# Kernel tuning notes

Hardware: AMD Instinct MI355X
Metric: run time of the kernel (lower is better)

The kernel has to match this reference:

```python
import jax, jax.numpy as jnp
import numpy as np

T, B, D, H = 2048, 64, 256, 256
DROPOUT = 0.3  # eval-mode recurrent dropout -> scalar scale (1 - dropout) on gate inputs


def setup_inputs() -> dict:
    key = jax.random.key(0)
    ks = jax.random.split(key, 5)
    x = jax.random.normal(ks[0], (T, B, D), dtype=jnp.float32)
    # variable sequence lengths, sorted descending (PackedSequence convention), min 1
    lengths = jnp.sort(jax.random.randint(ks[1], (B,), 1, T + 1))[::-1].astype(jnp.int64)
    # stacked gate weights, gate order i, f, c(g), o (matches bias_ih slicing)
    W = jax.random.normal(ks[2], (4 * H, D), dtype=jnp.float32) / np.sqrt(D).astype(np.float32)
    U = jax.random.normal(ks[3], (4 * H, H), dtype=jnp.float32) / np.sqrt(H).astype(np.float32)
    b_ih = jnp.zeros((4 * H,), jnp.float32).at[H:2 * H].set(1.0)  # forget-gate bias = 1
    b_hh = jnp.zeros((4 * H,), jnp.float32)
    return {"x": x, "lengths": lengths, "W": W, "U": U, "b_ih": b_ih, "b_hh": b_hh}


def reference(x, lengths, W, U, b_ih, b_hh):
    p = jnp.float32(1.0 - DROPOUT)
    Tn, Bn, _ = x.shape
    Hn = U.shape[1]
    b = b_ih + b_hh  # fused bias, shape [4H]
    t_idx = jnp.arange(Tn)

    def step(carry, inp):
        h, c = carry
        x_t, t = inp                      # x_t: [B, D]
        active = (t < lengths)[:, None]   # [B, 1] bool: sequence still running
        gates = (x_t * p) @ W.T + (h * p) @ U.T + b  # [B, 4H]
        i_g, f_g, g_g, o_g = jnp.split(gates, 4, axis=-1)
        i_t = jax.nn.sigmoid(i_g)
        f_t = jax.nn.sigmoid(f_g)
        o_t = jax.nn.sigmoid(o_g)
        c_new = f_t * c + i_t * jnp.tanh(g_g)
        h_new = o_t * jnp.tanh(c_new)
        # inactive rows keep their final state (packed-sequence semantics)
        h = jnp.where(active, h_new, h)
        c = jnp.where(active, c_new, c)
        out = jnp.where(active, h_new, jnp.float32(0.0))
        return (h, c), out

    init = (jnp.zeros((Bn, Hn), x.dtype), jnp.zeros((Bn, Hn), x.dtype))
    (h_n, c_n), outputs = jax.lax.scan(step, init, (x, t_idx))
    return outputs, h_n, c_n
```

## Files before the change

kernel.cpp:

```cpp
#include <hip/hip_runtime.h>


#define T_STEPS 2048
#define BATCH   64
#define DIM     256
#define HID     256
#define PKEEP   0.7f
#define RPG     16
#define TCHUNK  32
#define REGION_U32 (RPG * HID * 2)
#define PLANE_U32  (4 * REGION_U32)
#define XEL     (T_STEPS * BATCH * DIM)

typedef __attribute__((ext_vector_type(8))) short s16x8;
typedef __attribute__((ext_vector_type(4))) float f32x4;
typedef __attribute__((ext_vector_type(4))) unsigned int u32x4;
typedef __attribute__((ext_vector_type(2))) unsigned int u32x2;
typedef unsigned int u32;
typedef unsigned short u16;

#define HBUF_OFF 4096
#define BIG_OFF  (1 << 20)
#define ZERO_INTS (2 * PLANE_U32)

#define HISEL 0x07060302u
#define LOSEL 0x05040100u

__device__ __forceinline__ u16 f2bf_rne(float f) {
  unsigned x = __float_as_uint(f);
  return (u16)((x + 0x7fffu + ((x >> 16) & 1u)) >> 16);
}
__device__ __forceinline__ float bf2f(u16 u) { return __uint_as_float(((unsigned)u) << 16); }
__device__ __forceinline__ float sigm(float v) { return 1.0f / (1.0f + __expf(-v)); }
__device__ __forceinline__ float tanh_f(float v) {
  float e = __expf(-2.0f * fabsf(v));
  float r = (1.0f - e) / (1.0f + e);
  return v < 0.0f ? -r : r;
}
__device__ __forceinline__ u32 packbf(float v) {
  u32 uh = __float_as_uint(v) & 0xFFFF0000u;
  u32 lo = (u32)f2bf_rne(v - __uint_as_float(uh));
  return uh | lo;
}
__device__ __forceinline__ void dev_st_u32x2(u32* p, u32x2 v) {
  asm volatile("global_store_dwordx2 %0, %1, off sc0 sc1" :: "v"(p), "v"(v) : "memory");
}
__device__ __forceinline__ void gload_lds16(const u32* g, u32* lds) {
  __builtin_amdgcn_global_load_lds(
      (const __attribute__((address_space(1))) u32*)g,
      (__attribute__((address_space(3))) u32*)lds, 16, 0, 0);
}
__device__ __forceinline__ void unpack8(u32x4 a, u32x4 b, s16x8& hi, s16x8& lo) {
  u32x4 H, L;
  H[0] = __builtin_amdgcn_perm(a[1], a[0], HISEL);
  H[1] = __builtin_amdgcn_perm(a[3], a[2], HISEL);
  H[2] = __builtin_amdgcn_perm(b[1], b[0], HISEL);
  H[3] = __builtin_amdgcn_perm(b[3], b[2], HISEL);
  L[0] = __builtin_amdgcn_perm(a[1], a[0], LOSEL);
  L[1] = __builtin_amdgcn_perm(a[3], a[2], LOSEL);
  L[2] = __builtin_amdgcn_perm(b[1], b[0], LOSEL);
  L[3] = __builtin_amdgcn_perm(b[3], b[2], LOSEL);
  hi = __builtin_bit_cast(s16x8, H);
  lo = __builtin_bit_cast(s16x8, L);
}
__device__ __forceinline__ void xpose4(f32x4& a, bool b2, bool b3) {
  {
    int t0 = __builtin_amdgcn_ds_swizzle(__float_as_int(a[1]), 0x101F);
    int u0 = __builtin_amdgcn_ds_swizzle(__float_as_int(a[0]), 0x101F);
    int t1 = __builtin_amdgcn_ds_swizzle(__float_as_int(a[3]), 0x101F);
    int u1 = __builtin_amdgcn_ds_swizzle(__float_as_int(a[2]), 0x101F);
    float A0 = b2 ? __int_as_float(t0) : a[0];
    float A1 = b2 ? a[1] : __int_as_float(u0);
    float A2 = b2 ? __int_as_float(t1) : a[2];
    float A3 = b2 ? a[3] : __int_as_float(u1);
    a[0] = A0; a[1] = A1; a[2] = A2; a[3] = A3;
  }
  {
    int t0 = __builtin_amdgcn_ds_swizzle(__float_as_int(a[2]), 0x201F);
    int u0 = __builtin_amdgcn_ds_swizzle(__float_as_int(a[0]), 0x201F);
    int t1 = __builtin_amdgcn_ds_swizzle(__float_as_int(a[3]), 0x201F);
    int u1 = __builtin_amdgcn_ds_swizzle(__float_as_int(a[1]), 0x201F);
    float A0 = b3 ? __int_as_float(t0) : a[0];
    float A2 = b3 ? a[2] : __int_as_float(u0);
    float A1 = b3 ? __int_as_float(t1) : a[1];
    float A3 = b3 ? a[3] : __int_as_float(u1);
    a[0] = A0; a[1] = A1; a[2] = A2; a[3] = A3;
  }
}

__global__ void lstm_zero_ws(u32* __restrict__ p) {
  int i = blockIdx.x * 256 + threadIdx.x;
  if (i < ZERO_INTS) p[i] = 0;
}

__global__ void lstm_xpack(const float* __restrict__ x, u32* __restrict__ xpk) {
  long i = ((long)blockIdx.x * 256 + threadIdx.x) * 4;
  if (i >= (long)XEL) return;
  f32x4 v = *(const f32x4*)(x + i);
  u32x4 o;
#pragma unroll
  for (int e = 0; e < 4; ++e) o[e] = packbf(v[e] * PKEEP);
  *(u32x4*)(xpk + i) = o;
}

__global__ __launch_bounds__(256, 1) void lstm_gxp14(
    const float* __restrict__ x, const float* __restrict__ W,
    u32* __restrict__ Gxb) {
  const int tid = threadIdx.x;
  const int n = blockIdx.x & 15, m = (blockIdx.x >> 4) & 3;
  const int tc = blockIdx.x >> 6;
  const int t0 = tc * TCHUNK;
  const int lane = tid & 63, wave = tid >> 6;
  const int n16 = lane & 15, kgrp = lane >> 4;

  const int ghc_w = n * 16 + wave * 4 + (n16 & 3);
  const int grow = (n16 >> 2) * HID + ghc_w;
  s16x8 BWh[8], BWl[8];
#pragma unroll
  for (int ks = 0; ks < 8; ++ks) {
    const int base = grow * DIM + ks * 32 + kgrp * 8;
#pragma unroll
    for (int e = 0; e < 8; ++e) {
      float wv = W[base + e];
      u16 wh = f2bf_rne(wv);
      BWh[ks][e] = (short)wh;
      BWl[ks][e] = (short)f2bf_rne(wv - bf2f(wh));
    }
  }

  const bool b2 = (lane >> 2) & 1, b3 = (lane >> 3) & 1;
  const int row_l = kgrp * 4 + (n16 >> 2);
  const int gb = m * RPG + row_l;

  __shared__ u32 xstage[2][RPG * HID];

  {
    const int R = wave * 4;
    const long tb = (long)t0 * (BATCH * DIM) + (long)(m * RPG) * DIM;
#pragma unroll
    for (int r = 0; r < 4; ++r) {
      const long src = tb + (long)(R + r) * DIM + 4 * (lane ^ ((R + r) & 15));
      gload_lds16((const u32*)x + src, &xstage[0][(R + r) * HID]);
    }
  }

  for (int ti = 0; ti < TCHUNK; ++ti) {
    const int t = t0 + ti, par = ti & 1;
    asm volatile("s_waitcnt vmcnt(0)" ::: "memory");
    __builtin_amdgcn_sched_barrier(0);
    __syncthreads();

    const int swz = n16 << 4;
    f32x4 ax = {0.f, 0.f, 0.f, 0.f};
#pragma unroll
    for (int ks = 0; ks < 8; ++ks) {
      const int bb = n16 * 1024 + (kgrp * 8 + ks * 32) * 4;
      f32x4 f0 = *(const f32x4*)((const char*)xstage[par] + (bb ^ swz));
      f32x4 f1 = *(const f32x4*)((const char*)xstage[par] + ((bb + 16) ^ swz));
      s16x8 Xh, Xl;
#pragma unroll
      for (int e = 0; e < 8; ++e) {
        float v = (e < 4 ? f0[e] : f1[e - 4]) * PKEEP;
        unsigned hb = __float_as_uint(v) & 0xFFFF0000u;
        Xh[e] = (short)(hb >> 16);
        Xl[e] = (short)(u16)(__float_as_uint(v - __uint_as_float(hb)) >> 16);
      }
      ax = __builtin_amdgcn_mfma_f32_16x16x32_bf16(Xh, BWh[ks], ax, 0, 0, 0);
      ax = __builtin_amdgcn_mfma_f32_16x16x32_bf16(Xl, BWh[ks], ax, 0, 0, 0);
      ax = __builtin_amdgcn_mfma_f32_16x16x32_bf16(Xh, BWl[ks], ax, 0, 0, 0);
    }

    f32x4 g4 = ax;
    xpose4(g4, b2, b3);

    u32x2 pv;
    pv[0] = ((u32)f2bf_rne(g4[0]) << 16) | (u32)f2bf_rne(g4[1]);
    pv[1] = ((u32)f2bf_rne(g4[2]) << 16) | (u32)f2bf_rne(g4[3]);
    *(u32x2*)(Gxb + ((long)(t * BATCH + gb)) * 512 + ghc_w * 2) = pv;

    if (ti + 1 < TCHUNK) {
      const int R = wave * 4;
      const long tb = (long)(t + 1) * (BATCH * DIM) + (long)(m * RPG) * DIM;
#pragma unroll
      for (int r = 0; r < 4; ++r) {
        const long src = tb + (long)(R + r) * DIM + 4 * (lane ^ ((R + r) & 15));
        gload_lds16((const u32*)x + src, &xstage[par ^ 1][(R + r) * HID]);
      }
    }
  }
}

__global__ __launch_bounds__(256, 1) void lstm_recur_v14(
    const float* __restrict__ x, const int* __restrict__ lens,
    const float* __restrict__ W, const float* __restrict__ U,
    const float* __restrict__ bih, const float* __restrict__ bhh,
    float* __restrict__ out, u32* __restrict__ hbuf, const u32* __restrict__ Gxb) {
  const int wg = blockIdx.x, tid = threadIdx.x;
  const int m = wg >> 4, n = wg & 15;
  const int lane = tid & 63, wave = tid >> 6;
  const int n16 = lane & 15, kgrp = lane >> 4;

  const int ghc_w = n * 16 + wave * 4 + (n16 & 3);
  const int grow = (n16 >> 2) * HID + ghc_w;
  s16x8 BUh[8], BUl[8];
#pragma unroll
  for (int ks = 0; ks < 8; ++ks) {
    const int base = grow * DIM + ks * 32 + kgrp * 8;
#pragma unroll
    for (int e = 0; e < 8; ++e) {
      float uv = U[base + e];
      u16 uh = f2bf_rne(uv);
      BUh[ks][e] = (short)uh;
      BUl[ks][e] = (short)f2bf_rne(uv - bf2f(uh));
    }
  }

  const bool b2 = (lane >> 2) & 1, b3 = (lane >> 3) & 1;
  const int row_l = kgrp * 4 + (n16 >> 2);
  const int gb = m * RPG + row_l;
  const float bi  = bih[0 * HID + ghc_w] + bhh[0 * HID + ghc_w];
  const float bfo = bih[1 * HID + ghc_w] + bhh[1 * HID + ghc_w];
  const float bg  = bih[2 * HID + ghc_w] + bhh[2 * HID + ghc_w];
  const float bo  = bih[3 * HID + ghc_w] + bhh[3 * HID + ghc_w];
  const int len = lens[gb];
  float hreg = 0.0f, creg = 0.0f;

  const int rh = tid >> 7, p = tid & 127;
  __shared__ u32 hstage[2][RPG * HID];

  u32x2 gxu = *(const u32x2*)(Gxb + ((long)gb) * 512 + ghc_w * 2);

  for (int t = 0; t < T_STEPS; ++t) {
    const int par = t & 1;

    u32x4 P[8];
    {
      const u32* rb = hbuf + par * PLANE_U32 + m * REGION_U32 + rh * (8 * 512) + p * 4;
      for (;;) {
#pragma unroll
        for (int j = 0; j < 8; ++j)
          asm volatile("global_load_dwordx4 %0, %1, off sc0 sc1"
                       : "=v"(P[j]) : "v"(rb + j * 512) : "memory");
        asm volatile("s_waitcnt vmcnt(0)" ::: "memory");
        if (t == 0) break;
        bool stale = false;
#pragma unroll
        for (int j = 0; j < 8; ++j)
          stale |= (P[j][1] != (u32)t) || (P[j][3] != (u32)t);
        if (!__any(stale)) break;
      }
    }
    __builtin_amdgcn_sched_barrier(0);

#pragma unroll
    for (int j = 0; j < 8; ++j) {
      const int row = rh * 8 + j;
      const int byte = (row * 1024 + p * 8) ^ (row << 4);
      u32x2 v = {P[j][0], P[j][2]};
      *(u32x2*)((char*)hstage[par] + byte) = v;
    }
    __syncthreads();

    const int swz = n16 << 4;
    f32x4 ah = {0.f, 0.f, 0.f, 0.f};
#pragma unroll
    for (int ks = 0; ks < 8; ++ks) {
      const int bb = n16 * 1024 + (kgrp * 8 + ks * 32) * 4;
      u32x4 h0 = *(const u32x4*)((const char*)hstage[par] + (bb ^ swz));
      u32x4 h1 = *(const u32x4*)((const char*)hstage[par] + ((bb + 16) ^ swz));
      s16x8 Hh, Hl;
      unpack8(h0, h1, Hh, Hl);
      ah = __builtin_amdgcn_mfma_f32_16x16x32_bf16(Hh, BUh[ks], ah, 0, 0, 0);
      ah = __builtin_amdgcn_mfma_f32_16x16x32_bf16(Hl, BUh[ks], ah, 0, 0, 0);
      ah = __builtin_amdgcn_mfma_f32_16x16x32_bf16(Hh, BUl[ks], ah, 0, 0, 0);
    }

    f32x4 g4 = ah;
    xpose4(g4, b2, b3);
    float gi = g4[0] + __uint_as_float(gxu[0] & 0xFFFF0000u) + bi;
    float gf = g4[1] + __uint_as_float(gxu[0] << 16)          + bfo;
    float gg = g4[2] + __uint_as_float(gxu[1] & 0xFFFF0000u) + bg;
    float go = g4[3] + __uint_as_float(gxu[1] << 16)          + bo;
    float it = sigm(gi), ft = sigm(gf), ot = sigm(go);
    float gt = tanh_f(gg);
    float cnew = ft * creg + it * gt;
    float hnew = ot * tanh_f(cnew);
    const bool act = (t < len);
    if (act) { creg = cnew; hreg = hnew; }
    {
      u32x2 pv = {packbf(hreg * PKEEP), (u32)(t + 1)};
      dev_st_u32x2(hbuf + (par ^ 1) * PLANE_U32 + m * REGION_U32 + row_l * 512 + ghc_w * 2, pv);
    }

    if (t + 1 < T_STEPS)
      gxu = *(const u32x2*)(Gxb + ((long)((t + 1) * BATCH + gb)) * 512 + ghc_w * 2);
    out[(long)t * (BATCH * HID) + gb * HID + ghc_w] = act ? hnew : 0.0f;

    asm volatile("s_waitcnt vmcnt(0)" ::: "memory");
    __builtin_amdgcn_sched_barrier(0);
  }

  out[(long)T_STEPS * (BATCH * HID) + gb * HID + ghc_w] = hreg;
  out[(long)T_STEPS * (BATCH * HID) + BATCH * HID + gb * HID + ghc_w] = creg;
}

template <int MODE>
__device__ __forceinline__ void recur_body8(
    const float* __restrict__ x, const int* __restrict__ lens,
    const float* __restrict__ W, const float* __restrict__ U,
    const float* __restrict__ bih, const float* __restrict__ bhh,
    float* __restrict__ out, u32* __restrict__ hbuf, const u32* __restrict__ xpk) {
  const int wg = blockIdx.x, tid = threadIdx.x;
  const int m = wg >> 4, n = wg & 15;
  const int lane = tid & 63, wave = tid >> 6;
  const int n16 = lane & 15, kgrp = lane >> 4;

  const int ghc_w = n * 16 + wave * 4 + (n16 & 3);
  const int grow = (n16 >> 2) * HID + ghc_w;
  s16x8 BUh[8], BUl[8], BWh[8], BWl[8];
#pragma unroll
  for (int ks = 0; ks < 8; ++ks) {
    const int base = grow * DIM + ks * 32 + kgrp * 8;
#pragma unroll
    for (int e = 0; e < 8; ++e) {
      float uv = U[base + e];
      u16 uh = f2bf_rne(uv);
      BUh[ks][e] = (short)uh;
      BUl[ks][e] = (short)f2bf_rne(uv - bf2f(uh));
      float wv = W[base + e];
      u16 wh = f2bf_rne(wv);
      BWh[ks][e] = (short)wh;
      BWl[ks][e] = (short)f2bf_rne(wv - bf2f(wh));
    }
  }

  const bool b2 = (lane >> 2) & 1, b3 = (lane >> 3) & 1;
  const int row_l = kgrp * 4 + (n16 >> 2);
  const int gb = m * RPG + row_l;
  const float bi  = bih[0 * HID + ghc_w] + bhh[0 * HID + ghc_w];
  const float bfo = bih[1 * HID + ghc_w] + bhh[1 * HID + ghc_w];
  const float bg  = bih[2 * HID + ghc_w] + bhh[2 * HID + ghc_w];
  const float bo  = bih[3 * HID + ghc_w] + bhh[3 * HID + ghc_w];
  const int len = lens[gb];
  float hreg = 0.0f, creg = 0.0f;

  const int rh = tid >> 7, p = tid & 127;

  __shared__ u32 hstage[2][RPG * HID];
  __shared__ u32 xstage[2][RPG * HID];

  {
    const int R = wave * 4;
    const long tb = (long)(m * RPG) * DIM;
#pragma unroll
    for (int r = 0; r < 4; ++r) {
      const long src = tb + (long)(R + r) * DIM + 4 * (lane ^ ((R + r) & 15));
      if constexpr (MODE == 0) gload_lds16(xpk + src, &xstage[0][(R + r) * HID]);
      else                     gload_lds16((const u32*)x + src, &xstage[0][(R + r) * HID]);
    }
  }

  for (int t = 0; t < T_STEPS; ++t) {
    const int par = t & 1;
    u32x4 P[8];
    {
      const u32* rb = hbuf + par * PLANE_U32 + m * REGION_U32 + rh * (8 * 512) + p * 4;
      for (;;) {
#pragma unroll
        for (int j = 0; j < 8; ++j)
          asm volatile("global_load_dwordx4 %0, %1, off sc0 sc1"
                       : "=v"(P[j]) : "v"(rb + j * 512) : "memory");
        asm volatile("s_waitcnt vmcnt(0)" ::: "memory");
        if (t == 0) break;
        bool stale = false;
#pragma unroll
        for (int j = 0; j < 8; ++j)
          stale |= (P[j][1] != (u32)t) || (P[j][3] != (u32)t);
        if (!__any(stale)) break;
      }
    }
    __builtin_amdgcn_sched_barrier(0);

#pragma unroll
    for (int j = 0; j < 8; ++j) {
      const int row = rh * 8 + j;
      const int byte = (row * 1024 + p * 8) ^ (row << 4);
      u32x2 v = {P[j][0], P[j][2]};
      *(u32x2*)((char*)hstage[par] + byte) = v;
    }
    __syncthreads();

    const int swz = n16 << 4;
    f32x4 ah = {0.f, 0.f, 0.f, 0.f}, ax = {0.f, 0.f, 0.f, 0.f};
#pragma unroll
    for (int ks = 0; ks < 8; ++ks) {
      const int bb = n16 * 1024 + (kgrp * 8 + ks * 32) * 4;
      u32x4 h0 = *(const u32x4*)((const char*)hstage[par] + (bb ^ swz));
      u32x4 h1 = *(const u32x4*)((const char*)hstage[par] + ((bb + 16) ^ swz));
      s16x8 Hh, Hl, Xh, Xl;
      unpack8(h0, h1, Hh, Hl);
      if constexpr (MODE == 0) {
        u32x4 x0 = *(const u32x4*)((const char*)xstage[par] + (bb ^ swz));
        u32x4 x1 = *(const u32x4*)((const char*)xstage[par] + ((bb + 16) ^ swz));
        unpack8(x0, x1, Xh, Xl);
      } else {
        f32x4 f0 = *(const f32x4*)((const char*)xstage[par] + (bb ^ swz));
        f32x4 f1 = *(const f32x4*)((const char*)xstage[par] + ((bb + 16) ^ swz));
#pragma unroll
        for (int e = 0; e < 8; ++e) {
          float v = (e < 4 ? f0[e] : f1[e - 4]) * PKEEP;
          unsigned hb = __float_as_uint(v) & 0xFFFF0000u;
          Xh[e] = (short)(hb >> 16);
          Xl[e] = (short)(u16)(__float_as_uint(v - __uint_as_float(hb)) >> 16);
        }
      }
      ah = __builtin_amdgcn_mfma_f32_16x16x32_bf16(Hh, BUh[ks], ah, 0, 0, 0);
      ax = __builtin_amdgcn_mfma_f32_16x16x32_bf16(Xh, BWh[ks], ax, 0, 0, 0);
      ah = __builtin_amdgcn_mfma_f32_16x16x32_bf16(Hl, BUh[ks], ah, 0, 0, 0);
      ax = __builtin_amdgcn_mfma_f32_16x16x32_bf16(Xl, BWh[ks], ax, 0, 0, 0);
      ah = __builtin_amdgcn_mfma_f32_16x16x32_bf16(Hh, BUl[ks], ah, 0, 0, 0);
      ax = __builtin_amdgcn_mfma_f32_16x16x32_bf16(Xh, BWl[ks], ax, 0, 0, 0);
    }

    f32x4 g4 = ah + ax;
    xpose4(g4, b2, b3);

    float gi = g4[0] + bi, gf = g4[1] + bfo, gg = g4[2] + bg, go = g4[3] + bo;
    float it = sigm(gi), ft = sigm(gf), ot = sigm(go);
    float gt = tanh_f(gg);
    float cnew = ft * creg + it * gt;
    float hnew = ot * tanh_f(cnew);
    const bool act = (t < len);
    if (act) { creg = cnew; hreg = hnew; }
    {
      u32x2 pv = {packbf(hreg * PKEEP), (u32)(t + 1)};
      dev_st_u32x2(hbuf + (par ^ 1) * PLANE_U32 + m * REGION_U32 + row_l * 512 + ghc_w * 2, pv);
    }

    if (t + 1 < T_STEPS) {
      const int R = wave * 4;
      const long tb = (long)(t + 1) * (BATCH * DIM) + (long)(m * RPG) * DIM;
#pragma unroll
      for (int r = 0; r < 4; ++r) {
        const long src = tb + (long)(R + r) * DIM + 4 * (lane ^ ((R + r) & 15));
        if constexpr (MODE == 0) gload_lds16(xpk + src, &xstage[par ^ 1][(R + r) * HID]);
        else                     gload_lds16((const u32*)x + src, &xstage[par ^ 1][(R + r) * HID]);
      }
    }
    out[(long)t * (BATCH * HID) + gb * HID + ghc_w] = act ? hnew : 0.0f;

    asm volatile("s_waitcnt vmcnt(0)" ::: "memory");
    __builtin_amdgcn_sched_barrier(0);
  }

  out[(long)T_STEPS * (BATCH * HID) + gb * HID + ghc_w] = hreg;
  out[(long)T_STEPS * (BATCH * HID) + BATCH * HID + gb * HID + ghc_w] = creg;
}

#define RECUR_PARAMS                                                          \
  const float* __restrict__ x, const int* __restrict__ lens,                  \
  const float* __restrict__ W, const float* __restrict__ U,                   \
  const float* __restrict__ bih, const float* __restrict__ bhh,               \
  float* __restrict__ out, u32* __restrict__ hbuf, const u32* __restrict__ xpk
#define RECUR_ARGS x, lens, W, U, bih, bhh, out, hbuf, xpk

__global__ __launch_bounds__(256, 1) void lstm_recur_v8_xpk(RECUR_PARAMS) { recur_body8<0>(RECUR_ARGS); }
__global__ __launch_bounds__(256, 1) void lstm_recur_v8_dir(RECUR_PARAMS) { recur_body8<1>(RECUR_ARGS); }

extern "C" void kernel_launch(void* const* d_in, const int* in_sizes, int n_in,
                              void* d_out, int out_size, void* d_ws, size_t ws_size,
                              hipStream_t stream) {
  const float* x   = (const float*)d_in[0];
  const int*   len = (const int*)d_in[1];
  const float* W   = (const float*)d_in[2];
  const float* U   = (const float*)d_in[3];
  const float* bih = (const float*)d_in[4];
  const float* bhh = (const float*)d_in[5];
  float* out = (float*)d_out;
  char*  ws  = (char*)d_ws;
  u32* hbuf = (u32*)(ws + HBUF_OFF);
  char* big = ws + BIG_OFF;

  lstm_zero_ws<<<dim3((ZERO_INTS + 255) / 256), dim3(256), 0, stream>>>(hbuf);

  const size_t need_gx = (size_t)BIG_OFF + (size_t)T_STEPS * BATCH * 512 * 4;
  const size_t need_xp = (size_t)BIG_OFF + (size_t)XEL * 4;
  if (ws_size >= need_gx) {
    u32* Gxb = (u32*)big;
    lstm_gxp14<<<dim3(64 * (T_STEPS / TCHUNK)), dim3(256), 0, stream>>>(x, W, Gxb);
    lstm_recur_v14<<<dim3(64), dim3(256), 0, stream>>>(x, len, W, U, bih, bhh, out, hbuf, Gxb);
  } else if (ws_size >= need_xp) {
    u32* xpk = (u32*)big;
    lstm_xpack<<<dim3(32768), dim3(256), 0, stream>>>(x, xpk);
    lstm_recur_v8_xpk<<<dim3(64), dim3(256), 0, stream>>>(x, len, W, U, bih, bhh, out, hbuf, xpk);
  } else {
    lstm_recur_v8_dir<<<dim3(64), dim3(256), 0, stream>>>(x, len, W, U, bih, bhh, out, hbuf, nullptr);
  }
}
```

Before: 4.975 ms.

## Halve recurrent workgroups by computing two hidden-column tiles per workgroup

The recurrent kernel now runs 32 workgroups instead of 64. Each one handles 32 hidden columns as two interleaved 16-column MFMA tiles, with U held in registers for both tiles. The goal is to cut the number of workgroups taking part in the per-step cross-workgroup h exchange and spin-wait, and to reuse each staged h tile for twice the MFMA work. The cost is doubled register pressure from the weight fragments, plus more serial MFMA and gate work per step on each workgroup.

```diff
diff --git a/kernel.cpp b/kernel.cpp
--- a/kernel.cpp
+++ b/kernel.cpp
@@ -190,45 +190,55 @@
   }
 }
 
-__global__ __launch_bounds__(256, 1) void lstm_recur_v14(
+__global__ __launch_bounds__(256, 1) void lstm_recur_v15(
     const float* __restrict__ x, const int* __restrict__ lens,
     const float* __restrict__ W, const float* __restrict__ U,
     const float* __restrict__ bih, const float* __restrict__ bhh,
     float* __restrict__ out, u32* __restrict__ hbuf, const u32* __restrict__ Gxb) {
   const int wg = blockIdx.x, tid = threadIdx.x;
-  const int m = wg >> 4, n = wg & 15;
+  const int m = wg >> 3, nb = wg & 7;
   const int lane = tid & 63, wave = tid >> 6;
   const int n16 = lane & 15, kgrp = lane >> 4;
 
-  const int ghc_w = n * 16 + wave * 4 + (n16 & 3);
-  const int grow = (n16 >> 2) * HID + ghc_w;
-  s16x8 BUh[8], BUl[8];
+  const int ghc0 = nb * 32 + wave * 4 + (n16 & 3);
+  const int ghc1 = ghc0 + 16;
+  s16x8 BU0h[8], BU0l[8], BU1h[8], BU1l[8];
 #pragma unroll
   for (int ks = 0; ks < 8; ++ks) {
-    const int base = grow * DIM + ks * 32 + kgrp * 8;
+    const int base0 = ((n16 >> 2) * HID + ghc0) * DIM + ks * 32 + kgrp * 8;
+    const int base1 = ((n16 >> 2) * HID + ghc1) * DIM + ks * 32 + kgrp * 8;
 #pragma unroll
     for (int e = 0; e < 8; ++e) {
-      float uv = U[base + e];
-      u16 uh = f2bf_rne(uv);
-      BUh[ks][e] = (short)uh;
-      BUl[ks][e] = (short)f2bf_rne(uv - bf2f(uh));
+      float u0 = U[base0 + e];
+      u16 h0 = f2bf_rne(u0);
+      BU0h[ks][e] = (short)h0;
+      BU0l[ks][e] = (short)f2bf_rne(u0 - bf2f(h0));
+      float u1 = U[base1 + e];
+      u16 h1 = f2bf_rne(u1);
+      BU1h[ks][e] = (short)h1;
+      BU1l[ks][e] = (short)f2bf_rne(u1 - bf2f(h1));
     }
   }
 
   const bool b2 = (lane >> 2) & 1, b3 = (lane >> 3) & 1;
   const int row_l = kgrp * 4 + (n16 >> 2);
   const int gb = m * RPG + row_l;
-  const float bi  = bih[0 * HID + ghc_w] + bhh[0 * HID + ghc_w];
-  const float bfo = bih[1 * HID + ghc_w] + bhh[1 * HID + ghc_w];
-  const float bg  = bih[2 * HID + ghc_w] + bhh[2 * HID + ghc_w];
-  const float bo  = bih[3 * HID + ghc_w] + bhh[3 * HID + ghc_w];
+  const float bi0  = bih[0 * HID + ghc0] + bhh[0 * HID + ghc0];
+  const float bf0  = bih[1 * HID + ghc0] + bhh[1 * HID + ghc0];
+  const float bg0  = bih[2 * HID + ghc0] + bhh[2 * HID + ghc0];
+  const float bo0  = bih[3 * HID + ghc0] + bhh[3 * HID + ghc0];
+  const float bi1  = bih[0 * HID + ghc1] + bhh[0 * HID + ghc1];
+  const float bf1  = bih[1 * HID + ghc1] + bhh[1 * HID + ghc1];
+  const float bg1  = bih[2 * HID + ghc1] + bhh[2 * HID + ghc1];
+  const float bo1  = bih[3 * HID + ghc1] + bhh[3 * HID + ghc1];
   const int len = lens[gb];
-  float hreg = 0.0f, creg = 0.0f;
+  float hreg0 = 0.f, creg0 = 0.f, hreg1 = 0.f, creg1 = 0.f;
 
   const int rh = tid >> 7, p = tid & 127;
   __shared__ u32 hstage[2][RPG * HID];
 
-  u32x2 gxu = *(const u32x2*)(Gxb + ((long)gb) * 512 + ghc_w * 2);
+  u32x2 gxu0 = *(const u32x2*)(Gxb + ((long)gb) * 512 + ghc0 * 2);
+  u32x2 gxu1 = *(const u32x2*)(Gxb + ((long)gb) * 512 + ghc1 * 2);
 
   for (int t = 0; t < T_STEPS; ++t) {
     const int par = t & 1;
@@ -262,7 +272,7 @@
     __syncthreads();
 
     const int swz = n16 << 4;
-    f32x4 ah = {0.f, 0.f, 0.f, 0.f};
+    f32x4 a0 = {0.f, 0.f, 0.f, 0.f}, a1 = {0.f, 0.f, 0.f, 0.f};
 #pragma unroll
     for (int ks = 0; ks < 8; ++ks) {
       const int bb = n16 * 1024 + (kgrp * 8 + ks * 32) * 4;
@@ -270,38 +280,65 @@
       u32x4 h1 = *(const u32x4*)((const char*)hstage[par] + ((bb + 16) ^ swz));
       s16x8 Hh, Hl;
       unpack8(h0, h1, Hh, Hl);
-      ah = __builtin_amdgcn_mfma_f32_16x16x32_bf16(Hh, BUh[ks], ah, 0, 0, 0);
-      ah = __builtin_amdgcn_mfma_f32_16x16x32_bf16(Hl, BUh[ks], ah, 0, 0, 0);
-      ah = __builtin_amdgcn_mfma_f32_16x16x32_bf16(Hh, BUl[ks], ah, 0, 0, 0);
-    }
-
-    f32x4 g4 = ah;
-    xpose4(g4, b2, b3);
-    float gi = g4[0] + __uint_as_float(gxu[0] & 0xFFFF0000u) + bi;
-    float gf = g4[1] + __uint_as_float(gxu[0] << 16)          + bfo;
-    float gg = g4[2] + __uint_as_float(gxu[1] & 0xFFFF0000u) + bg;
-    float go = g4[3] + __uint_as_float(gxu[1] << 16)          + bo;
-    float it = sigm(gi), ft = sigm(gf), ot = sigm(go);
-    float gt = tanh_f(gg);
-    float cnew = ft * creg + it * gt;
-    float hnew = ot * tanh_f(cnew);
+      a0 = __builtin_amdgcn_mfma_f32_16x16x32_bf16(Hh, BU0h[ks], a0, 0, 0, 0);
+      a1 = __builtin_amdgcn_mfma_f32_16x16x32_bf16(Hh, BU1h[ks], a1, 0, 0, 0);
+      a0 = __builtin_amdgcn_mfma_f32_16x16x32_bf16(Hl, BU0h[ks], a0, 0, 0, 0);
+      a1 = __builtin_amdgcn_mfma_f32_16x16x32_bf16(Hl, BU1h[ks], a1, 0, 0, 0);
+      a0 = __builtin_amdgcn_mfma_f32_16x16x32_bf16(Hh, BU0l[ks], a0, 0, 0, 0);
+      a1 = __builtin_amdgcn_mfma_f32_16x16x32_bf16(Hh, BU1l[ks], a1, 0, 0, 0);
+    }
+
     const bool act = (t < len);
-    if (act) { creg = cnew; hreg = hnew; }
+    float hnew0, hnew1;
     {
-      u32x2 pv = {packbf(hreg * PKEEP), (u32)(t + 1)};
-      dev_st_u32x2(hbuf + (par ^ 1) * PLANE_U32 + m * REGION_U32 + row_l * 512 + ghc_w * 2, pv);
-    }
-
-    if (t + 1 < T_STEPS)
-      gxu = *(const u32x2*)(Gxb + ((long)((t + 1) * BATCH + gb)) * 512 + ghc_w * 2);
-    out[(long)t * (BATCH * HID) + gb * HID + ghc_w] = act ? hnew : 0.0f;
+      f32x4 g4 = a0;
+      xpose4(g4, b2, b3);
+      float gi = g4[0] + __uint_as_float(gxu0[0] & 0xFFFF0000u) + bi0;
+      float gf = g4[1] + __uint_as_float(gxu0[0] << 16)          + bf0;
+      float gg = g4[2] + __uint_as_float(gxu0[1] & 0xFFFF0000u) + bg0;
+      float go = g4[3] + __uint_as_float(gxu0[1] << 16)          + bo0;
+      float it = sigm(gi), ft = sigm(gf), ot = sigm(go);
+      float gt = tanh_f(gg);
+      float cnew = ft * creg0 + it * gt;
+      float hn = ot * tanh_f(cnew);
+      if (act) { creg0 = cnew; hreg0 = hn; }
+      hnew0 = hn;
+      u32x2 pv = {packbf(hreg0 * PKEEP), (u32)(t + 1)};
+      dev_st_u32x2(hbuf + (par ^ 1) * PLANE_U32 + m * REGION_U32 + row_l * 512 + ghc0 * 2, pv);
+    }
+    {
+      f32x4 g4 = a1;
+      xpose4(g4, b2, b3);
+      float gi = g4[0] + __uint_as_float(gxu1[0] & 0xFFFF0000u) + bi1;
+      float gf = g4[1] + __uint_as_float(gxu1[0] << 16)          + bf1;
+      float gg = g4[2] + __uint_as_float(gxu1[1] & 0xFFFF0000u) + bg1;
+      float go = g4[3] + __uint_as_float(gxu1[1] << 16)          + bo1;
+      float it = sigm(gi), ft = sigm(gf), ot = sigm(go);
+      float gt = tanh_f(gg);
+      float cnew = ft * creg1 + it * gt;
+      float hn = ot * tanh_f(cnew);
+      if (act) { creg1 = cnew; hreg1 = hn; }
+      hnew1 = hn;
+      u32x2 pv = {packbf(hreg1 * PKEEP), (u32)(t + 1)};
+      dev_st_u32x2(hbuf + (par ^ 1) * PLANE_U32 + m * REGION_U32 + row_l * 512 + ghc1 * 2, pv);
+    }
+
+    if (t + 1 < T_STEPS) {
+      const long gxb = ((long)((t + 1) * BATCH + gb)) * 512;
+      gxu0 = *(const u32x2*)(Gxb + gxb + ghc0 * 2);
+      gxu1 = *(const u32x2*)(Gxb + gxb + ghc1 * 2);
+    }
+    out[(long)t * (BATCH * HID) + gb * HID + ghc0] = act ? hnew0 : 0.0f;
+    out[(long)t * (BATCH * HID) + gb * HID + ghc1] = act ? hnew1 : 0.0f;
 
     asm volatile("s_waitcnt vmcnt(0)" ::: "memory");
     __builtin_amdgcn_sched_barrier(0);
   }
 
-  out[(long)T_STEPS * (BATCH * HID) + gb * HID + ghc_w] = hreg;
-  out[(long)T_STEPS * (BATCH * HID) + BATCH * HID + gb * HID + ghc_w] = creg;
+  out[(long)T_STEPS * (BATCH * HID) + gb * HID + ghc0] = hreg0;
+  out[(long)T_STEPS * (BATCH * HID) + gb * HID + ghc1] = hreg1;
+  out[(long)T_STEPS * (BATCH * HID) + BATCH * HID + gb * HID + ghc0] = creg0;
+  out[(long)T_STEPS * (BATCH * HID) + BATCH * HID + gb * HID + ghc1] = creg1;
 }
 
 template <int MODE>
@@ -488,7 +525,7 @@
   if (ws_size >= need_gx) {
     u32* Gxb = (u32*)big;
     lstm_gxp14<<<dim3(64 * (T_STEPS / TCHUNK)), dim3(256), 0, stream>>>(x, W, Gxb);
-    lstm_recur_v14<<<dim3(64), dim3(256), 0, stream>>>(x, len, W, U, bih, bhh, out, hbuf, Gxb);
+    lstm_recur_v15<<<dim3(32), dim3(256), 0, stream>>>(x, len, W, U, bih, bhh, out, hbuf, Gxb);
   } else if (ws_size >= need_xp) {
     u32* xpk = (u32*)big;
     lstm_xpack<<<dim3(32768), dim3(256), 0, stream>>>(x, xpk);
```

New measurement: 5.859 ms. 17.8% more time.

## Fuse input projection and recurrence into one producer-consumer kernel with flags

Applied to the files above, without the earlier changes.

Replaces the separate input-projection kernel and recurrence kernel with one launch of 128 workgroups. 64 workgroups run the sequential recurrence while 64 producer workgroups compute the W·x gate contributions step by step. The producers signal progress through coherent per-tile flags, so the recurrence starts without waiting for the whole projection pass. The risks are spin-wait latency on the flags, the producers pacing the consumers, and a deadlock if the two roles are not co-resident on the device.

```diff
diff --git a/kernel.cpp b/kernel.cpp
--- a/kernel.cpp
+++ b/kernel.cpp
@@ -7,10 +7,11 @@
 #define HID     256
 #define PKEEP   0.7f
 #define RPG     16
-#define TCHUNK  32
 #define REGION_U32 (RPG * HID * 2)
 #define PLANE_U32  (4 * REGION_U32)
 #define XEL     (T_STEPS * BATCH * DIM)
+#define NH      64
+#define NX      64
 
 typedef __attribute__((ext_vector_type(8))) short s16x8;
 typedef __attribute__((ext_vector_type(4))) float f32x4;
@@ -19,9 +20,10 @@
 typedef unsigned int u32;
 typedef unsigned short u16;
 
-#define HBUF_OFF 4096
+#define XF_OFF   4096
+#define HBUF_OFF 16384
 #define BIG_OFF  (1 << 20)
-#define ZERO_INTS (2 * PLANE_U32)
+#define ZERO_U32 ((HBUF_OFF + 2 * PLANE_U32 * 4) / 4)
 
 #define HISEL 0x07060302u
 #define LOSEL 0x05040100u
@@ -44,6 +46,19 @@
 }
 __device__ __forceinline__ void dev_st_u32x2(u32* p, u32x2 v) {
   asm volatile("global_store_dwordx2 %0, %1, off sc0 sc1" :: "v"(p), "v"(v) : "memory");
+}
+__device__ __forceinline__ void coh_st_i32(int* p, int v) {
+  asm volatile("global_store_dword %0, %1, off sc0 sc1" :: "v"(p), "v"(v) : "memory");
+}
+__device__ __forceinline__ int coh_ld_i32(const int* p) {
+  int v;
+  asm volatile("global_load_dword %0, %1, off sc0 sc1" : "=v"(v) : "v"(p) : "memory");
+  return v;
+}
+__device__ __forceinline__ u32x2 coh_ld_u32x2(const u32* p) {
+  u32x2 v;
+  asm volatile("global_load_dwordx2 %0, %1, off sc0 sc1" : "=v"(v) : "v"(p) : "memory");
+  return v;
 }
 __device__ __forceinline__ void gload_lds16(const u32* g, u32* lds) {
   __builtin_amdgcn_global_load_lds(
@@ -90,7 +105,7 @@
 
 __global__ void lstm_zero_ws(u32* __restrict__ p) {
   int i = blockIdx.x * 256 + threadIdx.x;
-  if (i < ZERO_INTS) p[i] = 0;
+  if (i < ZERO_U32) p[i] = 0;
 }
 
 __global__ void lstm_xpack(const float* __restrict__ x, u32* __restrict__ xpk) {
@@ -103,14 +118,12 @@
   *(u32x4*)(xpk + i) = o;
 }
 
-__global__ __launch_bounds__(256, 1) void lstm_gxp14(
+__device__ __forceinline__ void x_role(
     const float* __restrict__ x, const float* __restrict__ W,
-    u32* __restrict__ Gxb) {
-  const int tid = threadIdx.x;
-  const int n = blockIdx.x & 15, m = (blockIdx.x >> 4) & 3;
-  const int tc = blockIdx.x >> 6;
-  const int t0 = tc * TCHUNK;
-  const int lane = tid & 63, wave = tid >> 6;
+    u32* __restrict__ Gxb, int* __restrict__ xf, u32* smem) {
+  const int bx = blockIdx.x - NH;
+  const int m = bx >> 4, n = bx & 15;
+  const int tid = threadIdx.x, lane = tid & 63, wave = tid >> 6;
   const int n16 = lane & 15, kgrp = lane >> 4;
 
   const int ghc_w = n * 16 + wave * 4 + (n16 & 3);
@@ -127,36 +140,35 @@
       BWl[ks][e] = (short)f2bf_rne(wv - bf2f(wh));
     }
   }
-
   const bool b2 = (lane >> 2) & 1, b3 = (lane >> 3) & 1;
   const int row_l = kgrp * 4 + (n16 >> 2);
   const int gb = m * RPG + row_l;
-
-  __shared__ u32 xstage[2][RPG * HID];
+  int* flagp = xf + (m * 16 + n) * 16;
 
   {
     const int R = wave * 4;
-    const long tb = (long)t0 * (BATCH * DIM) + (long)(m * RPG) * DIM;
+    const long tb = (long)(m * RPG) * DIM;
 #pragma unroll
     for (int r = 0; r < 4; ++r) {
       const long src = tb + (long)(R + r) * DIM + 4 * (lane ^ ((R + r) & 15));
-      gload_lds16((const u32*)x + src, &xstage[0][(R + r) * HID]);
-    }
-  }
-
-  for (int ti = 0; ti < TCHUNK; ++ti) {
-    const int t = t0 + ti, par = ti & 1;
+      gload_lds16((const u32*)x + src, smem + (R + r) * HID);
+    }
+  }
+
+  for (int t = 0; t < T_STEPS; ++t) {
+    const int par = t & 1;
     asm volatile("s_waitcnt vmcnt(0)" ::: "memory");
     __builtin_amdgcn_sched_barrier(0);
     __syncthreads();
 
     const int swz = n16 << 4;
+    const char* xs = (const char*)smem + par * (RPG * HID * 4);
     f32x4 ax = {0.f, 0.f, 0.f, 0.f};
 #pragma unroll
     for (int ks = 0; ks < 8; ++ks) {
       const int bb = n16 * 1024 + (kgrp * 8 + ks * 32) * 4;
-      f32x4 f0 = *(const f32x4*)((const char*)xstage[par] + (bb ^ swz));
-      f32x4 f1 = *(const f32x4*)((const char*)xstage[par] + ((bb + 16) ^ swz));
+      f32x4 f0 = *(const f32x4*)(xs + (bb ^ swz));
+      f32x4 f1 = *(const f32x4*)(xs + ((bb + 16) ^ swz));
       s16x8 Xh, Xl;
 #pragma unroll
       for (int e = 0; e < 8; ++e) {
@@ -172,29 +184,31 @@
 
     f32x4 g4 = ax;
     xpose4(g4, b2, b3);
-
     u32x2 pv;
     pv[0] = ((u32)f2bf_rne(g4[0]) << 16) | (u32)f2bf_rne(g4[1]);
     pv[1] = ((u32)f2bf_rne(g4[2]) << 16) | (u32)f2bf_rne(g4[3]);
-    *(u32x2*)(Gxb + ((long)(t * BATCH + gb)) * 512 + ghc_w * 2) = pv;
-
-    if (ti + 1 < TCHUNK) {
+    dev_st_u32x2(Gxb + ((long)(t * BATCH + gb)) * 512 + ghc_w * 2, pv);
+
+    asm volatile("s_waitcnt vmcnt(0)" ::: "memory");
+    __syncthreads();
+    if (tid == 0) coh_st_i32(flagp, t + 1);
+    if (t + 1 < T_STEPS) {
       const int R = wave * 4;
       const long tb = (long)(t + 1) * (BATCH * DIM) + (long)(m * RPG) * DIM;
 #pragma unroll
       for (int r = 0; r < 4; ++r) {
         const long src = tb + (long)(R + r) * DIM + 4 * (lane ^ ((R + r) & 15));
-        gload_lds16((const u32*)x + src, &xstage[par ^ 1][(R + r) * HID]);
+        gload_lds16((const u32*)x + src, smem + (par ^ 1) * (RPG * HID) + (R + r) * HID);
       }
     }
   }
 }
 
-__global__ __launch_bounds__(256, 1) void lstm_recur_v14(
-    const float* __restrict__ x, const int* __restrict__ lens,
-    const float* __restrict__ W, const float* __restrict__ U,
+__device__ __forceinline__ void h_role(
+    const int* __restrict__ lens, const float* __restrict__ U,
     const float* __restrict__ bih, const float* __restrict__ bhh,
-    float* __restrict__ out, u32* __restrict__ hbuf, const u32* __restrict__ Gxb) {
+    float* __restrict__ out, u32* __restrict__ hbuf,
+    const u32* __restrict__ Gxb, const int* __restrict__ xf, u32* smem) {
   const int wg = blockIdx.x, tid = threadIdx.x;
   const int m = wg >> 4, n = wg & 15;
   const int lane = tid & 63, wave = tid >> 6;
@@ -226,12 +240,20 @@
   float hreg = 0.0f, creg = 0.0f;
 
   const int rh = tid >> 7, p = tid & 127;
-  __shared__ u32 hstage[2][RPG * HID];
-
-  u32x2 gxu = *(const u32x2*)(Gxb + ((long)gb) * 512 + ghc_w * 2);
+  const int* flagp = xf + (m * 16 + n) * 16;
+  int f = 0;
 
   for (int t = 0; t < T_STEPS; ++t) {
     const int par = t & 1;
+
+    if (f < t + 1) {
+      do {
+        f = coh_ld_i32(flagp);
+        asm volatile("s_waitcnt vmcnt(0)" ::: "memory");
+        __builtin_amdgcn_sched_barrier(0);
+      } while (f < t + 1);
+    }
+    u32x2 gxu = coh_ld_u32x2(Gxb + ((long)(t * BATCH + gb)) * 512 + ghc_w * 2);
 
     u32x4 P[8];
     {
@@ -252,12 +274,13 @@
     }
     __builtin_amdgcn_sched_barrier(0);
 
+    char* hs = (char*)smem + par * (RPG * HID * 4);
 #pragma unroll
     for (int j = 0; j < 8; ++j) {
       const int row = rh * 8 + j;
       const int byte = (row * 1024 + p * 8) ^ (row << 4);
       u32x2 v = {P[j][0], P[j][2]};
-      *(u32x2*)((char*)hstage[par] + byte) = v;
+      *(u32x2*)(hs + byte) = v;
     }
     __syncthreads();
 
@@ -266,8 +289,8 @@
 #pragma unroll
     for (int ks = 0; ks < 8; ++ks) {
       const int bb = n16 * 1024 + (kgrp * 8 + ks * 32) * 4;
-      u32x4 h0 = *(const u32x4*)((const char*)hstage[par] + (bb ^ swz));
-      u32x4 h1 = *(const u32x4*)((const char*)hstage[par] + ((bb + 16) ^ swz));
+      u32x4 h0 = *(const u32x4*)(hs + (bb ^ swz));
+      u32x4 h1 = *(const u32x4*)(hs + ((bb + 16) ^ swz));
       s16x8 Hh, Hl;
       unpack8(h0, h1, Hh, Hl);
       ah = __builtin_amdgcn_mfma_f32_16x16x32_bf16(Hh, BUh[ks], ah, 0, 0, 0);
@@ -292,9 +315,8 @@
       dev_st_u32x2(hbuf + (par ^ 1) * PLANE_U32 + m * REGION_U32 + row_l * 512 + ghc_w * 2, pv);
     }
 
-    if (t + 1 < T_STEPS)
-      gxu = *(const u32x2*)(Gxb + ((long)((t + 1) * BATCH + gb)) * 512 + ghc_w * 2);
     out[(long)t * (BATCH * HID) + gb * HID + ghc_w] = act ? hnew : 0.0f;
+    if (t + 1 < T_STEPS) f = coh_ld_i32(flagp);
 
     asm volatile("s_waitcnt vmcnt(0)" ::: "memory");
     __builtin_amdgcn_sched_barrier(0);
@@ -302,6 +324,17 @@
 
   out[(long)T_STEPS * (BATCH * HID) + gb * HID + ghc_w] = hreg;
   out[(long)T_STEPS * (BATCH * HID) + BATCH * HID + gb * HID + ghc_w] = creg;
+}
+
+__global__ __launch_bounds__(256, 1) void lstm_fused_v16(
+    const float* __restrict__ x, const int* __restrict__ lens,
+    const float* __restrict__ W, const float* __restrict__ U,
+    const float* __restrict__ bih, const float* __restrict__ bhh,
+    float* __restrict__ out, u32* __restrict__ hbuf,
+    u32* __restrict__ Gxb, int* __restrict__ xf) {
+  __shared__ u32 smem[2 * RPG * HID];
+  if (blockIdx.x < NH) h_role(lens, U, bih, bhh, out, hbuf, Gxb, xf, smem);
+  else                 x_role(x, W, Gxb, xf, smem);
 }
 
 template <int MODE>
@@ -478,17 +511,18 @@
   const float* bhh = (const float*)d_in[5];
   float* out = (float*)d_out;
   char*  ws  = (char*)d_ws;
+  int* xf   = (int*)(ws + XF_OFF);
   u32* hbuf = (u32*)(ws + HBUF_OFF);
   char* big = ws + BIG_OFF;
 
-  lstm_zero_ws<<<dim3((ZERO_INTS + 255) / 256), dim3(256), 0, stream>>>(hbuf);
+  lstm_zero_ws<<<dim3((ZERO_U32 + 255) / 256), dim3(256), 0, stream>>>((u32*)ws);
 
   const size_t need_gx = (size_t)BIG_OFF + (size_t)T_STEPS * BATCH * 512 * 4;
   const size_t need_xp = (size_t)BIG_OFF + (size_t)XEL * 4;
   if (ws_size >= need_gx) {
     u32* Gxb = (u32*)big;
-    lstm_gxp14<<<dim3(64 * (T_STEPS / TCHUNK)), dim3(256), 0, stream>>>(x, W, Gxb);
-    lstm_recur_v14<<<dim3(64), dim3(256), 0, stream>>>(x, len, W, U, bih, bhh, out, hbuf, Gxb);
+    lstm_fused_v16<<<dim3(NH + NX), dim3(256), 0, stream>>>(x, len, W, U, bih, bhh,
+                                                            out, hbuf, Gxb, xf);
   } else if (ws_size >= need_xp) {
     u32* xpk = (u32*)big;
     lstm_xpack<<<dim3(32768), dim3(256), 0, stream>>>(x, xpk);
```

Result: faster. 4.513 ms (-9.3%).
